# Kernel optimization log

Hardware: AMD Instinct MI355X
Metric: run time of the kernel (lower is better)

The kernel has to match this reference:

```python
import jax, jax.numpy as jnp
import numpy as np

BATCH, SEQ = 1, 2048
D_MODEL, N_HEADS, D_HEAD = 2048, 16, 128
ROTARY_DIM = 128
N_CTX = 2048
EPS = 1e-5
IGNORE = -100000.0
ATTN_SCALE = float(np.sqrt(D_HEAD))  # use_attn_scale=True, no layer-idx scaling
ROTARY_BASE = 10000.0


def _ln_pre(x):
    # LayerNormPre: center and normalize, no learned scale/bias
    x = x - x.mean(axis=-1, keepdims=True)
    scale = jnp.sqrt((x * x).mean(axis=-1, keepdims=True) + EPS)
    return x / scale


def _sin_cos_rotary(rotary_dim, n_ctx, base=ROTARY_BASE):
    pos = jnp.arange(n_ctx, dtype=jnp.float32)
    dim = jnp.arange(rotary_dim // 2, dtype=jnp.float32)
    freq = base ** (dim / (rotary_dim / 2))
    freq = jnp.repeat(freq, 2)  # einops.repeat 'd -> (d 2)' (interleaved)
    angles = pos[:, None] / freq[None, :]  # [n_ctx, rotary_dim]
    return jnp.sin(angles), jnp.cos(angles)


def _rotate_every_two(x):
    x1 = x[..., 0::2]
    x2 = x[..., 1::2]
    return jnp.stack([-x2, x1], axis=-1).reshape(x.shape)


def _apply_rotary(x, sin, cos):
    # x: [batch, pos, head, d_head]
    n_pos = x.shape[1]
    x_rot = x[..., :ROTARY_DIM]
    x_pass = x[..., ROTARY_DIM:]
    c = cos[:n_pos][:, None, :]  # [pos, 1, rotary_dim] broadcasts over head
    s = sin[:n_pos][:, None, :]
    x_rotated = x_rot * c + _rotate_every_two(x_rot) * s
    return jnp.concatenate([x_rotated, x_pass], axis=-1)


def setup_inputs() -> dict:
    key = jax.random.key(0)
    ks = jax.random.split(key, 6)
    init_std = 0.02
    return {
        "resid_pre": jax.random.normal(ks[0], (BATCH, SEQ, D_MODEL), jnp.float32),
        "W_Q": jax.random.normal(ks[1], (N_HEADS, D_MODEL, D_HEAD), jnp.float32) * init_std,
        "W_K": jax.random.normal(ks[2], (N_HEADS, D_MODEL, D_HEAD), jnp.float32) * init_std,
        "W_V": jax.random.normal(ks[3], (N_HEADS, D_MODEL, D_HEAD), jnp.float32) * init_std,
        "W_O": jax.random.normal(ks[4], (N_HEADS, D_HEAD, D_MODEL), jnp.float32) * init_std,
        "b_Q": jnp.zeros((N_HEADS, D_HEAD), jnp.float32),
        "b_K": jnp.zeros((N_HEADS, D_HEAD), jnp.float32),
        "b_V": jnp.zeros((N_HEADS, D_HEAD), jnp.float32),
        "b_O": jnp.zeros((D_MODEL,), jnp.float32),
    }


def reference(resid_pre, W_Q, W_K, W_V, W_O, b_Q, b_K, b_V, b_O):
    sin, cos = _sin_cos_rotary(ROTARY_DIM, N_CTX)
    xn = _ln_pre(resid_pre)  # LayerNormPre applied to resid_pre for q, k, v
    q = jnp.einsum("bpd,hde->bphe", xn, W_Q) + b_Q
    k = jnp.einsum("bpd,hde->bphe", xn, W_K) + b_K
    v = jnp.einsum("bpd,hde->bphe", xn, W_V) + b_V
    q = _apply_rotary(q, sin, cos)
    k = _apply_rotary(k, sin, cos)
    # attn_scores: [batch, head, query_pos, key_pos]
    scores = jnp.einsum("bqhe,bkhe->bhqk", q, k) / ATTN_SCALE
    n_pos = resid_pre.shape[1]
    causal = jnp.tril(jnp.ones((n_pos, n_pos), dtype=bool))
    scores = jnp.where(causal, scores, jnp.float32(IGNORE))
    attn = jax.nn.softmax(scores, axis=-1)
    z = jnp.einsum("bkhe,bhqk->bqhe", v, attn)
    out = jnp.einsum("bqhe,hed->bqd", z, W_O) + b_O
    return out
```

## Files before the change

kernel.cpp:

```cpp
#include <hip/hip_runtime.h>
#include <hip/hip_bf16.h>

#define SEQ    2048
#define DM     2048
#define NH     16
#define DH     128
#define EPS    1e-5f
#define SCALE_INV 0.08838834764831845f

typedef unsigned short u16;
typedef u16  u16x4  __attribute__((ext_vector_type(4)));
typedef u16  u16x8  __attribute__((ext_vector_type(8)));
typedef __bf16 bf16x8 __attribute__((ext_vector_type(8)));
typedef float f32x4 __attribute__((ext_vector_type(4)));

__device__ __forceinline__ u16 f2bf(float f) {
    unsigned int u = __builtin_bit_cast(unsigned int, f);
    u += 0x7fffu + ((u >> 16) & 1u);
    return (u16)(u >> 16);
}
__device__ __forceinline__ bf16x8 as_bf(u16x8 v) { return __builtin_bit_cast(bf16x8, v); }

__device__ __forceinline__ void gload16(const u16* g, u16* l) {
    __builtin_amdgcn_global_load_lds(
        (const __attribute__((address_space(1))) unsigned int*)g,
        (__attribute__((address_space(3))) unsigned int*)l, 16, 0, 0);
}

#define VMCNT(N) asm volatile("s_waitcnt vmcnt(" #N ")" ::: "memory")
#define LGKMCNT0 asm volatile("s_waitcnt lgkmcnt(0)" ::: "memory")
#define SCHEDBAR __builtin_amdgcn_sched_barrier(0)
#define BARRIER  __builtin_amdgcn_s_barrier()

__global__ void rope_kernel(float2* __restrict__ tab) {
    int i = threadIdx.x;
    int pos = blockIdx.x;
    float freq = powf(10000.f, (float)i * (1.f / 64.f));
    float ang = (float)pos / freq;
    tab[pos * 64 + i] = make_float2(sinf(ang), cosf(ang));
}

__global__ __launch_bounds__(256) void ln_kernel(const float* __restrict__ x,
                                                 u16* __restrict__ xn) {
    int row = blockIdx.x, t = threadIdx.x;
    const float* xr = x + (size_t)row * DM;
    float4 v0 = *(const float4*)(xr + t * 4);
    float4 v1 = *(const float4*)(xr + 1024 + t * 4);
    float s = v0.x + v0.y + v0.z + v0.w + v1.x + v1.y + v1.z + v1.w;
    float q = v0.x*v0.x + v0.y*v0.y + v0.z*v0.z + v0.w*v0.w
            + v1.x*v1.x + v1.y*v1.y + v1.z*v1.z + v1.w*v1.w;
    #pragma unroll
    for (int o = 32; o; o >>= 1) { s += __shfl_xor(s, o); q += __shfl_xor(q, o); }
    __shared__ float ss[4], qq[4];
    if ((t & 63) == 0) { ss[t >> 6] = s; qq[t >> 6] = q; }
    __syncthreads();
    s = ss[0] + ss[1] + ss[2] + ss[3];
    q = qq[0] + qq[1] + qq[2] + qq[3];
    float mean = s * (1.f / DM);
    float var  = q * (1.f / DM) - mean * mean;
    float rstd = rsqrtf(var + EPS);
    u16* orow = xn + (size_t)row * DM;
    u16x4 o0 = { f2bf((v0.x-mean)*rstd), f2bf((v0.y-mean)*rstd),
                 f2bf((v0.z-mean)*rstd), f2bf((v0.w-mean)*rstd) };
    u16x4 o1 = { f2bf((v1.x-mean)*rstd), f2bf((v1.y-mean)*rstd),
                 f2bf((v1.z-mean)*rstd), f2bf((v1.w-mean)*rstd) };
    *(u16x4*)(orow + t * 4) = o0;
    *(u16x4*)(orow + 1024 + t * 4) = o1;
}

__global__ __launch_bounds__(256) void transpose_qkv(const float* __restrict__ WQ,
                                                     const float* __restrict__ WK,
                                                     const float* __restrict__ WV,
                                                     u16* __restrict__ out) {
    int z = blockIdx.z, which = z >> 4, h = z & 15;
    const float* in = ((which == 0) ? WQ : (which == 1) ? WK : WV) + (size_t)h * DM * DH;
    u16* o = out + (size_t)z * DM * DH;
    int r0 = blockIdx.y * 64, c0 = blockIdx.x * 64;
    __shared__ u16 tile[64][65];
    int t = threadIdx.x;
    #pragma unroll
    for (int it = 0; it < 4; ++it) {
        int idx = t + it * 256;
        int rr = idx >> 4, cc = (idx & 15) * 4;
        float4 v = *(const float4*)(in + (size_t)(r0 + rr) * DH + c0 + cc);
        tile[rr][cc+0] = f2bf(v.x); tile[rr][cc+1] = f2bf(v.y);
        tile[rr][cc+2] = f2bf(v.z); tile[rr][cc+3] = f2bf(v.w);
    }
    __syncthreads();
    #pragma unroll
    for (int it = 0; it < 4; ++it) {
        int idx = t + it * 256;
        int oc = idx >> 4, orr = (idx & 15) * 4;
        u16x4 w = { tile[orr+0][oc], tile[orr+1][oc], tile[orr+2][oc], tile[orr+3][oc] };
        *(u16x4*)(o + (size_t)(c0 + oc) * DM + r0 + orr) = w;
    }
}

__global__ __launch_bounds__(256) void transpose_wo(const float* __restrict__ in,
                                                    u16* __restrict__ out) {
    int r0 = blockIdx.y * 64, c0 = blockIdx.x * 64;
    __shared__ u16 tile[64][65];
    int t = threadIdx.x;
    #pragma unroll
    for (int it = 0; it < 4; ++it) {
        int idx = t + it * 256;
        int rr = idx >> 4, cc = (idx & 15) * 4;
        float4 v = *(const float4*)(in + (size_t)(r0 + rr) * DM + c0 + cc);
        tile[rr][cc+0] = f2bf(v.x); tile[rr][cc+1] = f2bf(v.y);
        tile[rr][cc+2] = f2bf(v.z); tile[rr][cc+3] = f2bf(v.w);
    }
    __syncthreads();
    #pragma unroll
    for (int it = 0; it < 4; ++it) {
        int idx = t + it * 256;
        int oc = idx >> 4, orr = (idx & 15) * 4;
        u16x4 w = { tile[orr+0][oc], tile[orr+1][oc], tile[orr+2][oc], tile[orr+3][oc] };
        *(u16x4*)(out + (size_t)(c0 + oc) * DM + r0 + orr) = w;
    }
}

__global__ __launch_bounds__(512, 2) void gemm_qkv(const u16* __restrict__ Xn,
                                                   const u16* __restrict__ Wt,
                                                   const float* __restrict__ bQ,
                                                   const float* __restrict__ bK,
                                                   const float* __restrict__ bV,
                                                   const float2* __restrict__ rope,
                                                   u16* __restrict__ qkv) {
    __shared__ u16 As[2][256 * 64], Bs[2][256 * 64];
    int id = blockIdx.x;
    int swz = (id & 7) * 24 + (id >> 3);
    int bx = swz & 7, by = swz >> 3;
    int m0 = bx * 256, n0 = by * 256;

    int t = threadIdx.x, lane = t & 63, wid = t >> 6;
    int wr = wid >> 2, wc = wid & 3;
    int cl = lane & 15, g = lane >> 4;

    auto stage = [&](int buf, int kt) {
        const u16* xa = Xn + (size_t)kt * 64;
        const u16* xb = Wt + (size_t)kt * 64;
        #pragma unroll
        for (int j = 0; j < 4; ++j) {
            int idx = t + j * 512;
            int row = idx >> 3;
            int slotS = (idx & 7) ^ (row & 7);
            gload16(xa + (size_t)(m0 + row) * DM + slotS * 8, &As[buf][idx * 8]);
            gload16(xb + (size_t)(n0 + row) * DM + slotS * 8, &Bs[buf][idx * 8]);
        }
    };

    f32x4 acc[8][4] = {};
    stage(0, 0);
    VMCNT(0);
    BARRIER;

    for (int kt = 0; kt < 32; ++kt) {
        int p = kt & 1;
        bool more = (kt + 1 < 32);
        bf16x8 bfr[4][2], af[4][2];
        #pragma unroll
        for (int nj = 0; nj < 4; ++nj)
            #pragma unroll
            for (int kk = 0; kk < 2; ++kk) {
                int row = wc * 64 + nj * 16 + cl;
                int s = (kk * 4 + g) ^ (row & 7);
                bfr[nj][kk] = as_bf(*(const u16x8*)&Bs[p][row * 64 + s * 8]);
            }
        #pragma unroll
        for (int mi = 0; mi < 4; ++mi)
            #pragma unroll
            for (int kk = 0; kk < 2; ++kk) {
                int row = wr * 128 + mi * 16 + cl;
                int s = (kk * 4 + g) ^ (row & 7);
                af[mi][kk] = as_bf(*(const u16x8*)&As[p][row * 64 + s * 8]);
            }
        if (more) stage(p ^ 1, kt + 1);
        __builtin_amdgcn_s_setprio(1);
        #pragma unroll
        for (int mi = 0; mi < 4; ++mi)
            #pragma unroll
            for (int nj = 0; nj < 4; ++nj)
                #pragma unroll
                for (int kk = 0; kk < 2; ++kk)
                    acc[mi][nj] = __builtin_amdgcn_mfma_f32_16x16x32_bf16(af[mi][kk], bfr[nj][kk], acc[mi][nj], 0, 0, 0);
        __builtin_amdgcn_s_setprio(0);
        #pragma unroll
        for (int mi = 0; mi < 4; ++mi)
            #pragma unroll
            for (int kk = 0; kk < 2; ++kk) {
                int row = wr * 128 + 64 + mi * 16 + cl;
                int s = (kk * 4 + g) ^ (row & 7);
                af[mi][kk] = as_bf(*(const u16x8*)&As[p][row * 64 + s * 8]);
            }
        __builtin_amdgcn_s_setprio(1);
        #pragma unroll
        for (int mi = 0; mi < 4; ++mi)
            #pragma unroll
            for (int nj = 0; nj < 4; ++nj)
                #pragma unroll
                for (int kk = 0; kk < 2; ++kk)
                    acc[4 + mi][nj] = __builtin_amdgcn_mfma_f32_16x16x32_bf16(af[mi][kk], bfr[nj][kk], acc[4 + mi][nj], 0, 0, 0);
        __builtin_amdgcn_s_setprio(0);
        VMCNT(0);
        SCHEDBAR;
        BARRIER;
    }

    int which = n0 >> 11;
    const float* bias = (which == 0) ? bQ : (which == 1) ? bK : bV;
    #pragma unroll
    for (int i = 0; i < 8; ++i)
        #pragma unroll
        for (int nj = 0; nj < 4; ++nj) {
            int eg = n0 + wc * 64 + nj * 16 + cl;
            int h = (eg >> 7) & 15;
            int e = eg & 127;
            float bb = bias[h * DH + e];
            int p0 = m0 + wr * 128 + i * 16 + g * 4;
            if (which == 2) {
                u16* vbase = qkv + 2ll * NH * SEQ * DH + (size_t)h * DH * SEQ;
                u16x4 o = { f2bf(acc[i][nj][0] + bb), f2bf(acc[i][nj][1] + bb),
                            f2bf(acc[i][nj][2] + bb), f2bf(acc[i][nj][3] + bb) };
                *(u16x4*)(vbase + (size_t)e * SEQ + p0) = o;
            } else {
                u16* outbase = qkv + ((size_t)which * 16 + h) * SEQ * DH;
                #pragma unroll
                for (int r = 0; r < 4; ++r) {
                    int pp = p0 + r;
                    float v = acc[i][nj][r] + bb;
                    float pv = __shfl_xor(v, 1);
                    float2 sc2 = rope[pp * 64 + (e >> 1)];
                    v = (e & 1) ? (v * sc2.y + pv * sc2.x) : (v * sc2.y - pv * sc2.x);
                    outbase[(size_t)pp * DH + e] = f2bf(v);
                }
            }
        }
}

__global__ __launch_bounds__(256) void flash_kernel(const u16* __restrict__ Qg,
                                                    const u16* __restrict__ Kg,
                                                    const u16* __restrict__ Vt,
                                                    u16* __restrict__ Zg) {
    __shared__ u16 kt[64 * 128];
    __shared__ u16 vt[128 * 64];
    __shared__ u16 pt[4][16 * 72];
    int h = blockIdx.x;
    int nQ = gridDim.y;
    int q0 = (nQ - 1 - blockIdx.y) * 64;
    int t = threadIdx.x, lane = t & 63, w = t >> 6;
    int cl = lane & 15, g = lane >> 4;
    int qw0 = q0 + w * 16;
    const size_t hs = (size_t)h * SEQ;

    bf16x8 qf[4];
    #pragma unroll
    for (int st = 0; st < 4; ++st)
        qf[st] = as_bf(*(const u16x8*)(Qg + (hs + qw0 + cl) * DH + st * 32 + g * 8));

    f32x4 acc[8] = {};
    float mrun[4] = { -3e38f, -3e38f, -3e38f, -3e38f };
    float lsum[4] = { 0.f, 0.f, 0.f, 0.f };

    u16x8 kreg[4], vreg[4];
    auto load_tile = [&](int kv0) {
        #pragma unroll
        for (int j = 0; j < 4; ++j) {
            int idx = t + j * 256;
            kreg[j] = *(const u16x8*)(Kg + (hs + kv0 + (idx >> 4)) * DH + (idx & 15) * 8);
            vreg[j] = *(const u16x8*)(Vt + ((size_t)h * DH + (idx >> 3)) * SEQ + kv0 + (idx & 7) * 8);
        }
    };
    auto store_tile = [&]() {
        #pragma unroll
        for (int j = 0; j < 4; ++j) {
            int idx = t + j * 256;
            int row = idx >> 4, slot = idx & 15;
            *(u16x8*)((char*)kt + row * 256 + ((slot ^ (row & 7)) * 16)) = kreg[j];
            int e = idx >> 3, ch = idx & 7;
            *(u16x8*)((char*)vt + e * 128 + ((ch ^ (e & 7)) * 16)) = vreg[j];
        }
    };

    load_tile(0);
    store_tile();

    for (int kv0 = 0; kv0 <= q0; kv0 += 64) {
        __syncthreads();
        bool more = (kv0 + 64 <= q0);
        if (more) load_tile(kv0 + 64);

        f32x4 sc[4] = {};
        #pragma unroll
        for (int st = 0; st < 4; ++st)
            #pragma unroll
            for (int c = 0; c < 4; ++c) {
                int row = c * 16 + cl;
                bf16x8 kf = as_bf(*(const u16x8*)((char*)kt + row * 256 + (((st * 4 + g) ^ (row & 7)) * 16)));
                sc[c] = __builtin_amdgcn_mfma_f32_16x16x32_bf16(qf[st], kf, sc[c], 0, 0, 0);
            }

        bool needmask = (kv0 + 63 > qw0);
        float pvv[4][4], tm[4];
        #pragma unroll
        for (int r = 0; r < 4; ++r) tm[r] = -3e38f;
        #pragma unroll
        for (int c = 0; c < 4; ++c) {
            int col = kv0 + c * 16 + cl;
            #pragma unroll
            for (int r = 0; r < 4; ++r) {
                int qrow = qw0 + g * 4 + r;
                float sval = sc[c][r] * SCALE_INV;
                if (needmask) sval = (col <= qrow) ? sval : -3e38f;
                pvv[c][r] = sval;
                tm[r] = fmaxf(tm[r], sval);
            }
        }
        #pragma unroll
        for (int m = 1; m <= 8; m <<= 1)
            #pragma unroll
            for (int r = 0; r < 4; ++r) tm[r] = fmaxf(tm[r], __shfl_xor(tm[r], m));
        float alpha[4], rs[4];
        #pragma unroll
        for (int r = 0; r < 4; ++r) {
            float mn = fmaxf(mrun[r], tm[r]);
            alpha[r] = __expf(mrun[r] - mn);
            mrun[r] = mn;
            rs[r] = 0.f;
        }
        #pragma unroll
        for (int c = 0; c < 4; ++c)
            #pragma unroll
            for (int r = 0; r < 4; ++r) {
                float p = __expf(pvv[c][r] - mrun[r]);
                pvv[c][r] = p;
                rs[r] += p;
            }
        #pragma unroll
        for (int m = 1; m <= 8; m <<= 1)
            #pragma unroll
            for (int r = 0; r < 4; ++r) rs[r] += __shfl_xor(rs[r], m);
        #pragma unroll
        for (int r = 0; r < 4; ++r) lsum[r] = lsum[r] * alpha[r] + rs[r];
        #pragma unroll
        for (int n = 0; n < 8; ++n)
            #pragma unroll
            for (int r = 0; r < 4; ++r) acc[n][r] *= alpha[r];

        #pragma unroll
        for (int c = 0; c < 4; ++c)
            #pragma unroll
            for (int r = 0; r < 4; ++r)
                pt[w][(g * 4 + r) * 72 + c * 16 + cl] = f2bf(pvv[c][r]);

        bf16x8 pa[2];
        #pragma unroll
        for (int ks = 0; ks < 2; ++ks)
            pa[ks] = as_bf(*(const u16x8*)((char*)&pt[w][0] + cl * 144 + ks * 64 + g * 16));
        #pragma unroll
        for (int n = 0; n < 8; ++n)
            #pragma unroll
            for (int ks = 0; ks < 2; ++ks) {
                int e = n * 16 + cl;
                bf16x8 vf = as_bf(*(const u16x8*)((char*)vt + e * 128 + (((ks * 4 + g) ^ (e & 7)) * 16)));
                acc[n] = __builtin_amdgcn_mfma_f32_16x16x32_bf16(pa[ks], vf, acc[n], 0, 0, 0);
            }

        if (!more) break;
        __syncthreads();
        store_tile();
    }

    float inv[4];
    #pragma unroll
    for (int r = 0; r < 4; ++r) inv[r] = 1.0f / lsum[r];
    #pragma unroll
    for (int n = 0; n < 8; ++n)
        #pragma unroll
        for (int r = 0; r < 4; ++r) {
            int q = qw0 + g * 4 + r;
            Zg[(hs + q) * DH + n * 16 + cl] = f2bf(acc[n][r] * inv[r]);
        }
}

__global__ __launch_bounds__(256) void gemm_out(const u16* __restrict__ Z,
                                                const u16* __restrict__ Wot,
                                                const float* __restrict__ bO,
                                                float* __restrict__ out) {
    __shared__ u16 As[2 * 128 * 32], Bs[2 * 128 * 32];
    int m0 = blockIdx.x * 128, n0 = blockIdx.y * 128;
    int t = threadIdx.x, lane = t & 63, w = t >> 6;
    int wr = w >> 1, wc = w & 1;
    int cl = lane & 15, g = lane >> 4;
    int swz = (cl >> 1) & 3;

    auto stage = [&](int buf, int k0) {
        u16* Ab = As + buf * (128 * 32);
        u16* Bb = Bs + buf * (128 * 32);
        int hh = k0 >> 7, e0 = k0 & 127;
        #pragma unroll
        for (int j = 0; j < 2; ++j) {
            int idx = t + j * 256;
            int row = idx >> 2, slot = idx & 3;
            int slotS = slot ^ ((row >> 1) & 3);
            gload16(Z + ((size_t)hh * SEQ + m0 + row) * DH + e0 + slotS * 8, Ab + idx * 8);
            gload16(Wot + (size_t)(n0 + row) * DM + k0 + slotS * 8, Bb + idx * 8);
        }
    };

    f32x4 acc[4][4] = {};
    stage(0, 0);
    int cur = 0;
    for (int k0 = 0; k0 < DM; k0 += 32) {
        bool more = (k0 + 32 < DM);
        if (more) {
            stage(cur ^ 1, k0 + 32);
            VMCNT(4);
        } else {
            VMCNT(0);
        }
        SCHEDBAR;
        BARRIER;
        const u16* Ac = As + cur * (128 * 32);
        const u16* Bc = Bs + cur * (128 * 32);
        bf16x8 af[4], bfr[4];
        #pragma unroll
        for (int i = 0; i < 4; ++i)
            af[i] = as_bf(*(const u16x8*)&Ac[(wr*64 + i*16 + cl) * 32 + (g ^ swz) * 8]);
        #pragma unroll
        for (int j = 0; j < 4; ++j)
            bfr[j] = as_bf(*(const u16x8*)&Bc[(wc*64 + j*16 + cl) * 32 + (g ^ swz) * 8]);
        #pragma unroll
        for (int i = 0; i < 4; ++i)
            #pragma unroll
            for (int j = 0; j < 4; ++j)
                acc[i][j] = __builtin_amdgcn_mfma_f32_16x16x32_bf16(af[i], bfr[j], acc[i][j], 0, 0, 0);
        LGKMCNT0;
        SCHEDBAR;
        BARRIER;
        cur ^= 1;
    }
    #pragma unroll
    for (int i = 0; i < 4; ++i)
        #pragma unroll
        for (int j = 0; j < 4; ++j) {
            int col = n0 + wc * 64 + j * 16 + cl;
            float bb = bO[col];
            #pragma unroll
            for (int r = 0; r < 4; ++r) {
                int p = m0 + wr * 64 + i * 16 + g * 4 + r;
                out[(size_t)p * DM + col] = acc[i][j][r] + bb;
            }
        }
}

extern "C" void kernel_launch(void* const* d_in, const int* in_sizes, int n_in,
                              void* d_out, int out_size, void* d_ws, size_t ws_size,
                              hipStream_t stream) {
    const float* resid = (const float*)d_in[0];
    const float* WQ = (const float*)d_in[1];
    const float* WK = (const float*)d_in[2];
    const float* WV = (const float*)d_in[3];
    const float* WO = (const float*)d_in[4];
    const float* bQ = (const float*)d_in[5];
    const float* bK = (const float*)d_in[6];
    const float* bV = (const float*)d_in[7];
    const float* bO = (const float*)d_in[8];
    float* out = (float*)d_out;
    char* ws = (char*)d_ws;

    float2* rope = (float2*)(ws);
    u16* xn   = (u16*)(ws + (1ll  << 20));
    u16* Wt   = (u16*)(ws + (9ll  << 20));
    u16* Wot  = (u16*)(ws + (33ll << 20));
    u16* qkv  = (u16*)(ws + (41ll << 20));
    u16* z    = (u16*)(ws + (65ll << 20));

    rope_kernel<<<SEQ, 64, 0, stream>>>(rope);
    ln_kernel<<<SEQ, 256, 0, stream>>>(resid, xn);

    transpose_qkv<<<dim3(2, 32, 48), 256, 0, stream>>>(WQ, WK, WV, Wt);
    transpose_wo<<<dim3(32, 32, 1), 256, 0, stream>>>(WO, Wot);

    gemm_qkv<<<192, 512, 0, stream>>>(xn, Wt, bQ, bK, bV, rope, qkv);

    const u16* Qg = qkv;
    const u16* Kg = qkv + 1ll * NH * SEQ * DH;
    const u16* Vt = qkv + 2ll * NH * SEQ * DH;
    flash_kernel<<<dim3(NH, SEQ / 64), 256, 0, stream>>>(Qg, Kg, Vt, z);

    gemm_out<<<dim3(16, 16), 256, 0, stream>>>(z, Wot, bO, out);
}
```

Measured before the change: 210.3 us.

## Transpose QK^T MFMA so each lane owns one query row; lazy softmax rescale

Swaps the MFMA operands for the score tile so each lane holds scores for a single query row. Row max and sum then need only two cross-lane shuffles instead of four per row. It also folds the log2(e) factor into the scale to use exp2, and skips rescaling the accumulator unless the running max grows by more than a threshold (wave-uniform check). P is packed into bf16 pairs and written to a swizzled LDS buffer with 64-bit stores, which cuts the number of LDS writes. The cost is some extra shuffles to redistribute alpha and the final 1/l to the accumulator layout.

```diff
diff --git a/kernel.cpp b/kernel.cpp
--- a/kernel.cpp
+++ b/kernel.cpp
@@ -7,6 +7,7 @@
 #define DH     128
 #define EPS    1e-5f
 #define SCALE_INV 0.08838834764831845f
+#define SC2LOG    0.12751744995f
 
 typedef unsigned short u16;
 typedef u16  u16x4  __attribute__((ext_vector_type(4)));
@@ -243,7 +244,7 @@
                                                     u16* __restrict__ Zg) {
     __shared__ u16 kt[64 * 128];
     __shared__ u16 vt[128 * 64];
-    __shared__ u16 pt[4][16 * 72];
+    __shared__ unsigned pt32[4 * 16 * 32];
     int h = blockIdx.x;
     int nQ = gridDim.y;
     int q0 = (nQ - 1 - blockIdx.y) * 64;
@@ -251,6 +252,8 @@
     int cl = lane & 15, g = lane >> 4;
     int qw0 = q0 + w * 16;
     const size_t hs = (size_t)h * SEQ;
+    unsigned* ptw = pt32 + w * (16 * 32) + cl * 32;
+    int swv = (cl & 7) << 1;
 
     bf16x8 qf[4];
     #pragma unroll
@@ -258,8 +261,7 @@
         qf[st] = as_bf(*(const u16x8*)(Qg + (hs + qw0 + cl) * DH + st * 32 + g * 8));
 
     f32x4 acc[8] = {};
-    float mrun[4] = { -3e38f, -3e38f, -3e38f, -3e38f };
-    float lsum[4] = { 0.f, 0.f, 0.f, 0.f };
+    float mrun = -3e38f, lsum = 0.f;
 
     u16x8 kreg[4], vreg[4];
     auto load_tile = [&](int kv0) {
@@ -296,66 +298,65 @@
             for (int c = 0; c < 4; ++c) {
                 int row = c * 16 + cl;
                 bf16x8 kf = as_bf(*(const u16x8*)((char*)kt + row * 256 + (((st * 4 + g) ^ (row & 7)) * 16)));
-                sc[c] = __builtin_amdgcn_mfma_f32_16x16x32_bf16(qf[st], kf, sc[c], 0, 0, 0);
+                sc[c] = __builtin_amdgcn_mfma_f32_16x16x32_bf16(kf, qf[st], sc[c], 0, 0, 0);
             }
 
         bool needmask = (kv0 + 63 > qw0);
-        float pvv[4][4], tm[4];
-        #pragma unroll
-        for (int r = 0; r < 4; ++r) tm[r] = -3e38f;
+        int qrow = qw0 + cl;
+        float pf[4][4];
+        float tm = -3e38f;
+        #pragma unroll
+        for (int c = 0; c < 4; ++c)
+            #pragma unroll
+            for (int r = 0; r < 4; ++r) {
+                int kvq = kv0 + c * 16 + g * 4 + r;
+                float sval = sc[c][r] * SC2LOG;
+                if (needmask) sval = (kvq <= qrow) ? sval : -3e38f;
+                pf[c][r] = sval;
+                tm = fmaxf(tm, sval);
+            }
+        tm = fmaxf(tm, __shfl_xor(tm, 16));
+        tm = fmaxf(tm, __shfl_xor(tm, 32));
+
+        if (!__all(tm <= mrun + 12.f)) {
+            float mn = fmaxf(mrun, tm);
+            float alpha = exp2f(mrun - mn);
+            mrun = mn;
+            lsum *= alpha;
+            float aR[4];
+            #pragma unroll
+            for (int r = 0; r < 4; ++r) aR[r] = __shfl(alpha, g * 4 + r);
+            #pragma unroll
+            for (int n = 0; n < 8; ++n)
+                #pragma unroll
+                for (int r = 0; r < 4; ++r) acc[n][r] *= aR[r];
+        }
+        float rs = 0.f;
+        #pragma unroll
+        for (int c = 0; c < 4; ++c)
+            #pragma unroll
+            for (int r = 0; r < 4; ++r) {
+                float e2 = exp2f(pf[c][r] - mrun);
+                pf[c][r] = e2;
+                rs += e2;
+            }
+        rs += __shfl_xor(rs, 16);
+        rs += __shfl_xor(rs, 32);
+        lsum += rs;
+
         #pragma unroll
         for (int c = 0; c < 4; ++c) {
-            int col = kv0 + c * 16 + cl;
-            #pragma unroll
-            for (int r = 0; r < 4; ++r) {
-                int qrow = qw0 + g * 4 + r;
-                float sval = sc[c][r] * SCALE_INV;
-                if (needmask) sval = (col <= qrow) ? sval : -3e38f;
-                pvv[c][r] = sval;
-                tm[r] = fmaxf(tm[r], sval);
-            }
-        }
-        #pragma unroll
-        for (int m = 1; m <= 8; m <<= 1)
-            #pragma unroll
-            for (int r = 0; r < 4; ++r) tm[r] = fmaxf(tm[r], __shfl_xor(tm[r], m));
-        float alpha[4], rs[4];
-        #pragma unroll
-        for (int r = 0; r < 4; ++r) {
-            float mn = fmaxf(mrun[r], tm[r]);
-            alpha[r] = __expf(mrun[r] - mn);
-            mrun[r] = mn;
-            rs[r] = 0.f;
-        }
-        #pragma unroll
-        for (int c = 0; c < 4; ++c)
-            #pragma unroll
-            for (int r = 0; r < 4; ++r) {
-                float p = __expf(pvv[c][r] - mrun[r]);
-                pvv[c][r] = p;
-                rs[r] += p;
-            }
-        #pragma unroll
-        for (int m = 1; m <= 8; m <<= 1)
-            #pragma unroll
-            for (int r = 0; r < 4; ++r) rs[r] += __shfl_xor(rs[r], m);
-        #pragma unroll
-        for (int r = 0; r < 4; ++r) lsum[r] = lsum[r] * alpha[r] + rs[r];
-        #pragma unroll
-        for (int n = 0; n < 8; ++n)
-            #pragma unroll
-            for (int r = 0; r < 4; ++r) acc[n][r] *= alpha[r];
-
-        #pragma unroll
-        for (int c = 0; c < 4; ++c)
-            #pragma unroll
-            for (int r = 0; r < 4; ++r)
-                pt[w][(g * 4 + r) * 72 + c * 16 + cl] = f2bf(pvv[c][r]);
-
+            unsigned lo = (unsigned)f2bf(pf[c][0]) | ((unsigned)f2bf(pf[c][1]) << 16);
+            unsigned hi = (unsigned)f2bf(pf[c][2]) | ((unsigned)f2bf(pf[c][3]) << 16);
+            int u = (c * 4 + g) ^ swv;
+            *(unsigned long long*)(ptw + u * 2) =
+                (unsigned long long)lo | ((unsigned long long)hi << 32);
+        }
         bf16x8 pa[2];
         #pragma unroll
         for (int ks = 0; ks < 2; ++ks)
-            pa[ks] = as_bf(*(const u16x8*)((char*)&pt[w][0] + cl * 144 + ks * 64 + g * 16));
+            pa[ks] = as_bf(*(const u16x8*)(ptw + ((ks * 8 + g * 2) ^ swv) * 2));
+
         #pragma unroll
         for (int n = 0; n < 8; ++n)
             #pragma unroll
@@ -370,15 +371,16 @@
         store_tile();
     }
 
-    float inv[4];
-    #pragma unroll
-    for (int r = 0; r < 4; ++r) inv[r] = 1.0f / lsum[r];
+    float inv = 1.0f / lsum;
+    float invR[4];
+    #pragma unroll
+    for (int r = 0; r < 4; ++r) invR[r] = __shfl(inv, g * 4 + r);
     #pragma unroll
     for (int n = 0; n < 8; ++n)
         #pragma unroll
         for (int r = 0; r < 4; ++r) {
             int q = qw0 + g * 4 + r;
-            Zg[(hs + q) * DH + n * 16 + cl] = f2bf(acc[n][r] * inv[r]);
+            Zg[(hs + q) * DH + n * 16 + cl] = f2bf(acc[n][r] * invR[r]);
         }
 }
 
```

Result: faster. 203.3 us (-3.3%).
